# Kernel optimization log

Measured on AMD Instinct MI355X. Metric: run time of the kernel, lower is better.

The kernel has to match this reference:

```python
import jax, jax.numpy as jnp
import numpy as np

T, B, V, E, H = 128, 32, 32000, 32, 16
KEEP = 0.8  # 1 - dropout_percent


def setup_inputs() -> dict:
    key = jax.random.key(0)
    ks = jax.random.split(key, 11)
    stdv = 1.0 / np.sqrt(H)  # init_params: uniform(-stdv, stdv) for ALL params (incl. embedding)
    u = lambda k, shape: jax.random.uniform(k, shape, jnp.float32, -stdv, stdv)
    return {
        "input_batch": jax.random.randint(ks[0], (T, B), 0, V),
        "embedding": u(ks[1], (V, E)),
        "W_ih_lr": u(ks[2], (E + H, H)),
        "b_ih_lr": u(ks[3], (1, H)),
        "W_ih_rl": u(ks[4], (E + H, H)),
        "b_ih_rl": u(ks[5], (1, H)),
        "W_ho": u(ks[6], (2 * H, V)),
        "b_ho": u(ks[7], (1, V)),
        "initial_hidden": u(ks[8], (1, H)),
        # pre-sampled inverted-dropout masks (torch samples np.random.binomial each step)
        "mask_lr": jax.random.bernoulli(ks[9], KEEP, (T, B, H)).astype(jnp.float32) / KEEP,
        "mask_rl": jax.random.bernoulli(ks[10], KEEP, (T, B, H)).astype(jnp.float32) / KEEP,
    }


def reference(input_batch, embedding, W_ih_lr, b_ih_lr, W_ih_rl, b_ih_rl,
              W_ho, b_ho, initial_hidden, mask_lr, mask_rl):
    seq_len, batch = input_batch.shape
    # torch uses initial_hidden.data -> no grad flows into initial_hidden
    h0 = jnp.broadcast_to(jax.lax.stop_gradient(initial_hidden), (batch, initial_hidden.shape[1]))

    def make_step(W, b):
        def step(h, xm):
            ix, m = xm
            w = embedding[ix]                                   # [B, E] gather
            h = jnp.tanh(jnp.concatenate([w, h], axis=1) @ W + b) * m
            return h, h
        return step

    # left-to-right: hLR[t+1] = state after consuming token t
    _, ys_lr = jax.lax.scan(make_step(W_ih_lr, b_ih_lr), h0, (input_batch, mask_lr))
    # right-to-left: hRL[t-1] = state after consuming token t-1 (tokens fed reversed)
    _, ys_rl = jax.lax.scan(make_step(W_ih_rl, b_ih_rl), h0, (input_batch[::-1], mask_rl[::-1]))

    hLR = jnp.concatenate([h0[None], ys_lr], axis=0)        # [T+1, B, H]
    hRL = jnp.concatenate([ys_rl[::-1], h0[None]], axis=0)  # [T+1, B, H]

    # prediction for position i uses hLR[i] (left ctx) and hRL[i+1] (right ctx)
    feats = jnp.concatenate([hLR[:-1], hRL[1:]], axis=-1)   # [T, B, 2H]
    logits = feats @ W_ho + b_ho                            # [T, B, V]
    return jax.nn.log_softmax(logits, axis=-1)
```

## Files before the change

### kernel.cpp

```cpp
#include <hip/hip_runtime.h>
#include <hip/hip_bf16.h>
#include <math.h>

#define T_ 128
#define B_ 32
#define V_ 32000
#define E_ 32
#define H_ 16
#define NSEG 20
#define SEGW 1600
#define NIT 25

typedef __attribute__((ext_vector_type(8))) short short8;
typedef __attribute__((ext_vector_type(4))) float f32x4;


__global__ __launch_bounds__(256) void xw_kernel(const int* __restrict__ ix,
                                                 const float* __restrict__ emb,
                                                 const float* __restrict__ W_lr,
                                                 const float* __restrict__ b_lr,
                                                 const float* __restrict__ W_rl,
                                                 const float* __restrict__ b_rl,
                                                 float* __restrict__ xw) {
    int idx = blockIdx.x * 256 + threadIdx.x;
    int j = idx & 15;
    int b = (idx >> 4) & 31;
    int t = (idx >> 9) & 127;
    int dir = idx >> 16;
    const float* W    = dir ? W_rl : W_lr;
    const float* bias = dir ? b_rl : b_lr;
    int tok = ix[t * B_ + b];
    const float* er = emb + (long)tok * E_;
    float acc = bias[j];
#pragma unroll
    for (int e = 0; e < E_; ++e) acc += er[e] * W[e * H_ + j];
    xw[idx] = acc;
}

__global__ __launch_bounds__(512) void scan_kernel(const float* __restrict__ xw,
                                                   const float* __restrict__ W_lr,
                                                   const float* __restrict__ W_rl,
                                                   const float* __restrict__ h0p,
                                                   const float* __restrict__ mask_lr,
                                                   const float* __restrict__ mask_rl,
                                                   __hip_bfloat16* __restrict__ featsB) {
    int dir = blockIdx.x;
    int tid = threadIdx.x;
    int lane = tid & 63;
    int j = lane & 15;
    int b = tid >> 4;
    int base = lane & 48;
    const float* W    = dir ? W_rl : W_lr;
    const float* mask = dir ? mask_rl : mask_lr;
    const float* xwd  = xw + dir * (T_ * B_ * H_);
    float Wh[16];
#pragma unroll
    for (int k = 0; k < 16; ++k) Wh[k] = W[(E_ + k) * H_ + j];
    float h = h0p[j];
    if (dir == 0) featsB[(0 * B_ + b) * 32 + j] = __float2bfloat16(h);
    else          featsB[((T_ - 1) * B_ + b) * 32 + 16 + j] = __float2bfloat16(h);

    float x0[4], m0[4], x1[4], m1[4];
#define LOADCH(XB, MB, CH)                                                 \
    _Pragma("unroll")                                                      \
    for (int u = 0; u < 4; ++u) {                                          \
        int t = (CH) * 4 + u;                                              \
        int tt = dir ? (T_ - 1 - t) : t;                                   \
        XB[u] = xwd[tt * (B_ * H_) + tid];                                 \
        MB[u] = mask[tt * (B_ * H_) + tid];                                \
    }
#define STEPS(XB, MB, CH)                                                  \
    _Pragma("unroll")                                                      \
    for (int u = 0; u < 4; ++u) {                                          \
        int t = (CH) * 4 + u;                                              \
        float a0 = XB[u], a1 = 0.f, a2 = 0.f, a3 = 0.f;                    \
        _Pragma("unroll")                                                  \
        for (int k = 0; k < 16; k += 4) {                                  \
            a0 += __shfl(h, base + k,     64) * Wh[k];                     \
            a1 += __shfl(h, base + k + 1, 64) * Wh[k + 1];                 \
            a2 += __shfl(h, base + k + 2, 64) * Wh[k + 2];                 \
            a3 += __shfl(h, base + k + 3, 64) * Wh[k + 3];                 \
        }                                                                  \
        float ax = (a0 + a1) + (a2 + a3);                                  \
        float ex = __expf(2.f * ax);                                       \
        float th = 1.f - 2.f * __builtin_amdgcn_rcpf(ex + 1.f);            \
        float hn = th * MB[u];                                             \
        h = hn;                                                            \
        int p = dir ? (T_ - 2 - t) : (t + 1);                              \
        if (p >= 0 && p < T_)                                              \
            featsB[(p * B_ + b) * 32 + dir * 16 + j] = __float2bfloat16(hn); \
    }
    LOADCH(x0, m0, 0)
#pragma unroll 1
    for (int c = 0; c < 32; c += 2) {
        if (c + 1 < 32) { LOADCH(x1, m1, c + 1) }
        STEPS(x0, m0, c)
        if (c + 2 < 32) { LOADCH(x0, m0, c + 2) }
        STEPS(x1, m1, c + 1)
    }
#undef LOADCH
#undef STEPS
}

__global__ __launch_bounds__(256) void wt_kernel(const float* __restrict__ W_ho,
                                                 __hip_bfloat16* __restrict__ W_hoT) {
    int c = blockIdx.x * 256 + threadIdx.x;
    __hip_bfloat16 tmp[32];
#pragma unroll
    for (int k = 0; k < 32; ++k) tmp[k] = __float2bfloat16(W_ho[k * V_ + c]);
    short8* dst = (short8*)(W_hoT + c * 32);
    const short8* src = (const short8*)tmp;
#pragma unroll
    for (int q = 0; q < 4; ++q) dst[q] = src[q];
}


__global__ __launch_bounds__(256) void stats_kernel(const __hip_bfloat16* __restrict__ featsB,
                                                    const __hip_bfloat16* __restrict__ W_hoT,
                                                    const float* __restrict__ b_ho,
                                                    float* __restrict__ stats_part) {
    int wv = threadIdx.x >> 6, lane = threadIdx.x & 63;
    int rt = blockIdx.x * 4 + wv;
    int seg = blockIdx.y;
    int row0 = rt * 16;
    int p = lane & 15, kb = (lane >> 4) * 8, quad = (lane >> 4) << 2;
    short8 bfrag = *(const short8*)((const short*)featsB + (row0 + p) * 32 + kb);
    int cbase = seg * SEGW;
    const short* WA = (const short*)W_hoT;
    short8 a0n = *(const short8*)(WA + (cbase +  0 + p) * 32 + kb);
    short8 a1n = *(const short8*)(WA + (cbase + 16 + p) * 32 + kb);
    short8 a2n = *(const short8*)(WA + (cbase + 32 + p) * 32 + kb);
    short8 a3n = *(const short8*)(WA + (cbase + 48 + p) * 32 + kb);
    float r0 = 0.f, r1 = 0.f, r2 = 0.f, r3 = 0.f;
#pragma unroll 1
    for (int it = 0; it < NIT; ++it) {
        short8 a0 = a0n, a1 = a1n, a2 = a2n, a3 = a3n;
        if (it < NIT - 1) {
            int cn = cbase + (it + 1) * 64;
            a0n = *(const short8*)(WA + (cn +  0 + p) * 32 + kb);
            a1n = *(const short8*)(WA + (cn + 16 + p) * 32 + kb);
            a2n = *(const short8*)(WA + (cn + 32 + p) * 32 + kb);
            a3n = *(const short8*)(WA + (cn + 48 + p) * 32 + kb);
        }
        int c0 = cbase + it * 64;
        f32x4 b40 = *(const f32x4*)(b_ho + c0 +  0 + quad);
        f32x4 b41 = *(const f32x4*)(b_ho + c0 + 16 + quad);
        f32x4 b42 = *(const f32x4*)(b_ho + c0 + 32 + quad);
        f32x4 b43 = *(const f32x4*)(b_ho + c0 + 48 + quad);
        f32x4 lg0 = __builtin_amdgcn_mfma_f32_16x16x32_bf16(a0, bfrag, (f32x4){0.f,0.f,0.f,0.f}, 0, 0, 0);
        f32x4 lg1 = __builtin_amdgcn_mfma_f32_16x16x32_bf16(a1, bfrag, (f32x4){0.f,0.f,0.f,0.f}, 0, 0, 0);
        f32x4 lg2 = __builtin_amdgcn_mfma_f32_16x16x32_bf16(a2, bfrag, (f32x4){0.f,0.f,0.f,0.f}, 0, 0, 0);
        f32x4 lg3 = __builtin_amdgcn_mfma_f32_16x16x32_bf16(a3, bfrag, (f32x4){0.f,0.f,0.f,0.f}, 0, 0, 0);
        r0 += __expf(lg0[0] + b40[0]) + __expf(lg0[1] + b40[1]) +
              __expf(lg0[2] + b40[2]) + __expf(lg0[3] + b40[3]);
        r1 += __expf(lg1[0] + b41[0]) + __expf(lg1[1] + b41[1]) +
              __expf(lg1[2] + b41[2]) + __expf(lg1[3] + b41[3]);
        r2 += __expf(lg2[0] + b42[0]) + __expf(lg2[1] + b42[1]) +
              __expf(lg2[2] + b42[2]) + __expf(lg2[3] + b42[3]);
        r3 += __expf(lg3[0] + b43[0]) + __expf(lg3[1] + b43[1]) +
              __expf(lg3[2] + b43[2]) + __expf(lg3[3] + b43[3]);
    }
    float racc = (r0 + r1) + (r2 + r3);
    racc += __shfl_xor(racc, 16, 64);
    racc += __shfl_xor(racc, 32, 64);
    if (lane < 16) stats_part[(row0 + lane) * NSEG + seg] = racc;
}

__global__ __launch_bounds__(256) void lse_kernel(const float* __restrict__ stats_part,
                                                  float* __restrict__ lse) {
    int r = blockIdx.x * 256 + threadIdx.x;
    const float* sp = stats_part + r * NSEG;
    float s = 0.f;
#pragma unroll
    for (int i = 0; i < NSEG; ++i) s += sp[i];
    lse[r] = __logf(s);
}

__global__ __launch_bounds__(256) void out_kernel(const __hip_bfloat16* __restrict__ featsB,
                                                  const __hip_bfloat16* __restrict__ W_hoT,
                                                  const float* __restrict__ b_ho,
                                                  const float* __restrict__ lse,
                                                  float* __restrict__ out) {
    __shared__ float tile[4][16][68];
    int wv = threadIdx.x >> 6, lane = threadIdx.x & 63;
    int rt = blockIdx.x * 4 + wv;
    int seg = blockIdx.y;
    int row0 = rt * 16;
    int p = lane & 15, kb = (lane >> 4) * 8, quad = (lane >> 4) << 2;
    short8 bfrag = *(const short8*)((const short*)featsB + (row0 + p) * 32 + kb);
    float ls = lse[row0 + p];
    int cbase = seg * SEGW;
    const short* WA = (const short*)W_hoT;
    float* tw = &tile[wv][0][0];
    int rr = lane >> 4;
    int cc = (lane & 15) * 4;
    short8 a0n = *(const short8*)(WA + (cbase +  0 + p) * 32 + kb);
    short8 a1n = *(const short8*)(WA + (cbase + 16 + p) * 32 + kb);
    short8 a2n = *(const short8*)(WA + (cbase + 32 + p) * 32 + kb);
    short8 a3n = *(const short8*)(WA + (cbase + 48 + p) * 32 + kb);
#pragma unroll 1
    for (int it = 0; it < NIT; ++it) {
        short8 a0 = a0n, a1 = a1n, a2 = a2n, a3 = a3n;
        if (it < NIT - 1) {
            int cn = cbase + (it + 1) * 64;
            a0n = *(const short8*)(WA + (cn +  0 + p) * 32 + kb);
            a1n = *(const short8*)(WA + (cn + 16 + p) * 32 + kb);
            a2n = *(const short8*)(WA + (cn + 32 + p) * 32 + kb);
            a3n = *(const short8*)(WA + (cn + 48 + p) * 32 + kb);
        }
        int c0 = cbase + it * 64;
        f32x4 b40 = *(const f32x4*)(b_ho + c0 +  0 + quad);
        f32x4 b41 = *(const f32x4*)(b_ho + c0 + 16 + quad);
        f32x4 b42 = *(const f32x4*)(b_ho + c0 + 32 + quad);
        f32x4 b43 = *(const f32x4*)(b_ho + c0 + 48 + quad);
        f32x4 lg0 = __builtin_amdgcn_mfma_f32_16x16x32_bf16(a0, bfrag, (f32x4){0.f,0.f,0.f,0.f}, 0, 0, 0);
        f32x4 lg1 = __builtin_amdgcn_mfma_f32_16x16x32_bf16(a1, bfrag, (f32x4){0.f,0.f,0.f,0.f}, 0, 0, 0);
        f32x4 lg2 = __builtin_amdgcn_mfma_f32_16x16x32_bf16(a2, bfrag, (f32x4){0.f,0.f,0.f,0.f}, 0, 0, 0);
        f32x4 lg3 = __builtin_amdgcn_mfma_f32_16x16x32_bf16(a3, bfrag, (f32x4){0.f,0.f,0.f,0.f}, 0, 0, 0);
        *(f32x4*)(tw + p * 68 +  0 + quad) = lg0 + b40 - ls;
        *(f32x4*)(tw + p * 68 + 16 + quad) = lg1 + b41 - ls;
        *(f32x4*)(tw + p * 68 + 32 + quad) = lg2 + b42 - ls;
        *(f32x4*)(tw + p * 68 + 48 + quad) = lg3 + b43 - ls;
#pragma unroll
        for (int s = 0; s < 4; ++s) {
            int r = s * 4 + rr;
            f32x4 v = *(const f32x4*)(tw + r * 68 + cc);
            __builtin_nontemporal_store(v, (f32x4*)(out + (long)(row0 + r) * V_ + c0 + cc));
        }
    }
}

extern "C" void kernel_launch(void* const* d_in, const int* in_sizes, int n_in,
                              void* d_out, int out_size, void* d_ws, size_t ws_size,
                              hipStream_t stream) {
    const int*   ix      = (const int*)d_in[0];
    const float* emb     = (const float*)d_in[1];
    const float* W_lr    = (const float*)d_in[2];
    const float* b_lr    = (const float*)d_in[3];
    const float* W_rl    = (const float*)d_in[4];
    const float* b_rl    = (const float*)d_in[5];
    const float* W_ho    = (const float*)d_in[6];
    const float* b_ho    = (const float*)d_in[7];
    const float* h0      = (const float*)d_in[8];
    const float* mask_lr = (const float*)d_in[9];
    const float* mask_rl = (const float*)d_in[10];
    float* out = (float*)d_out;
    float* ws  = (float*)d_ws;

    float*           xw         = ws;
    __hip_bfloat16*  featsB     = (__hip_bfloat16*)(ws + 131072);
    __hip_bfloat16*  W_hoT      = (__hip_bfloat16*)(ws + 196608);
    float*           stats_part = ws + 708608;
    float*           lse        = ws + 790528;

    xw_kernel<<<512, 256, 0, stream>>>(ix, emb, W_lr, b_lr, W_rl, b_rl, xw);
    wt_kernel<<<125, 256, 0, stream>>>(W_ho, W_hoT);
    scan_kernel<<<2, 512, 0, stream>>>(xw, W_lr, W_rl, h0, mask_lr, mask_rl, featsB);
    stats_kernel<<<dim3(64, NSEG), 256, 0, stream>>>(featsB, W_hoT, b_ho, stats_part);
    lse_kernel<<<16, 256, 0, stream>>>(stats_part, lse);
    out_kernel<<<dim3(64, NSEG), 256, 0, stream>>>(featsB, W_hoT, b_ho, lse, out);
}
```

Before: 221.1 us.

## Split scan into per-wave blocks, fuse wt and lse, double rows in stats

The recurrent scan is split from 2 blocks of 512 threads into 16 single-wave blocks, one per direction and group of 4 batch rows, each run independently. The W_ho transpose runs as extra blocks of that same launch. The stats kernel now handles 32 rows per wave so each W_hoT fragment feeds two MFMAs. The lse kernel is removed: out_kernel sums the partial stats itself and stages the bias segment in shared memory. The intent is to cut launch count and serial latency in the scan, at the cost of redundant log-sum work in out_kernel and fewer stats blocks.

```diff
diff --git a/kernel.cpp b/kernel.cpp
--- a/kernel.cpp
+++ b/kernel.cpp
@@ -37,18 +37,31 @@
     xw[idx] = acc;
 }
 
-__global__ __launch_bounds__(512) void scan_kernel(const float* __restrict__ xw,
-                                                   const float* __restrict__ W_lr,
-                                                   const float* __restrict__ W_rl,
-                                                   const float* __restrict__ h0p,
-                                                   const float* __restrict__ mask_lr,
-                                                   const float* __restrict__ mask_rl,
-                                                   __hip_bfloat16* __restrict__ featsB) {
-    int dir = blockIdx.x;
-    int tid = threadIdx.x;
-    int lane = tid & 63;
+__global__ __launch_bounds__(64) void scanwt_kernel(const float* __restrict__ xw,
+                                                    const float* __restrict__ W_lr,
+                                                    const float* __restrict__ W_rl,
+                                                    const float* __restrict__ h0p,
+                                                    const float* __restrict__ mask_lr,
+                                                    const float* __restrict__ mask_rl,
+                                                    __hip_bfloat16* __restrict__ featsB,
+                                                    const float* __restrict__ W_ho,
+                                                    __hip_bfloat16* __restrict__ W_hoT) {
+    if (blockIdx.x >= 16) {
+        int c = (blockIdx.x - 16) * 64 + threadIdx.x;
+        __hip_bfloat16 tmp[32];
+#pragma unroll
+        for (int k = 0; k < 32; ++k) tmp[k] = __float2bfloat16(W_ho[k * V_ + c]);
+        short8* dst = (short8*)(W_hoT + c * 32);
+        const short8* src = (const short8*)tmp;
+#pragma unroll
+        for (int q = 0; q < 4; ++q) dst[q] = src[q];
+        return;
+    }
+    int lane = threadIdx.x;
+    int dir = blockIdx.x >> 3;
     int j = lane & 15;
-    int b = tid >> 4;
+    int b = (blockIdx.x & 7) * 4 + (lane >> 4);
+    int bi = b * 16 + j;
     int base = lane & 48;
     const float* W    = dir ? W_rl : W_lr;
     const float* mask = dir ? mask_rl : mask_lr;
@@ -66,8 +79,8 @@
     for (int u = 0; u < 4; ++u) {                                          \
         int t = (CH) * 4 + u;                                              \
         int tt = dir ? (T_ - 1 - t) : t;                                   \
-        XB[u] = xwd[tt * (B_ * H_) + tid];                                 \
-        MB[u] = mask[tt * (B_ * H_) + tid];                                \
+        XB[u] = xwd[tt * (B_ * H_) + bi];                                  \
+        MB[u] = mask[tt * (B_ * H_) + bi];                                 \
     }
 #define STEPS(XB, MB, CH)                                                  \
     _Pragma("unroll")                                                      \
@@ -102,18 +115,6 @@
 #undef STEPS
 }
 
-__global__ __launch_bounds__(256) void wt_kernel(const float* __restrict__ W_ho,
-                                                 __hip_bfloat16* __restrict__ W_hoT) {
-    int c = blockIdx.x * 256 + threadIdx.x;
-    __hip_bfloat16 tmp[32];
-#pragma unroll
-    for (int k = 0; k < 32; ++k) tmp[k] = __float2bfloat16(W_ho[k * V_ + c]);
-    short8* dst = (short8*)(W_hoT + c * 32);
-    const short8* src = (const short8*)tmp;
-#pragma unroll
-    for (int q = 0; q < 4; ++q) dst[q] = src[q];
-}
-
 
 __global__ __launch_bounds__(256) void stats_kernel(const __hip_bfloat16* __restrict__ featsB,
                                                     const __hip_bfloat16* __restrict__ W_hoT,
@@ -122,16 +123,17 @@
     int wv = threadIdx.x >> 6, lane = threadIdx.x & 63;
     int rt = blockIdx.x * 4 + wv;
     int seg = blockIdx.y;
-    int row0 = rt * 16;
+    int row0 = rt * 32;
     int p = lane & 15, kb = (lane >> 4) * 8, quad = (lane >> 4) << 2;
-    short8 bfrag = *(const short8*)((const short*)featsB + (row0 + p) * 32 + kb);
+    short8 bf0 = *(const short8*)((const short*)featsB + (row0 + p) * 32 + kb);
+    short8 bf1 = *(const short8*)((const short*)featsB + (row0 + 16 + p) * 32 + kb);
     int cbase = seg * SEGW;
     const short* WA = (const short*)W_hoT;
     short8 a0n = *(const short8*)(WA + (cbase +  0 + p) * 32 + kb);
     short8 a1n = *(const short8*)(WA + (cbase + 16 + p) * 32 + kb);
     short8 a2n = *(const short8*)(WA + (cbase + 32 + p) * 32 + kb);
     short8 a3n = *(const short8*)(WA + (cbase + 48 + p) * 32 + kb);
-    float r0 = 0.f, r1 = 0.f, r2 = 0.f, r3 = 0.f;
+    float ra = 0.f, rb = 0.f;
 #pragma unroll 1
     for (int it = 0; it < NIT; ++it) {
         short8 a0 = a0n, a1 = a1n, a2 = a2n, a3 = a3n;
@@ -147,49 +149,62 @@
         f32x4 b41 = *(const f32x4*)(b_ho + c0 + 16 + quad);
         f32x4 b42 = *(const f32x4*)(b_ho + c0 + 32 + quad);
         f32x4 b43 = *(const f32x4*)(b_ho + c0 + 48 + quad);
-        f32x4 lg0 = __builtin_amdgcn_mfma_f32_16x16x32_bf16(a0, bfrag, (f32x4){0.f,0.f,0.f,0.f}, 0, 0, 0);
-        f32x4 lg1 = __builtin_amdgcn_mfma_f32_16x16x32_bf16(a1, bfrag, (f32x4){0.f,0.f,0.f,0.f}, 0, 0, 0);
-        f32x4 lg2 = __builtin_amdgcn_mfma_f32_16x16x32_bf16(a2, bfrag, (f32x4){0.f,0.f,0.f,0.f}, 0, 0, 0);
-        f32x4 lg3 = __builtin_amdgcn_mfma_f32_16x16x32_bf16(a3, bfrag, (f32x4){0.f,0.f,0.f,0.f}, 0, 0, 0);
-        r0 += __expf(lg0[0] + b40[0]) + __expf(lg0[1] + b40[1]) +
-              __expf(lg0[2] + b40[2]) + __expf(lg0[3] + b40[3]);
-        r1 += __expf(lg1[0] + b41[0]) + __expf(lg1[1] + b41[1]) +
-              __expf(lg1[2] + b41[2]) + __expf(lg1[3] + b41[3]);
-        r2 += __expf(lg2[0] + b42[0]) + __expf(lg2[1] + b42[1]) +
-              __expf(lg2[2] + b42[2]) + __expf(lg2[3] + b42[3]);
-        r3 += __expf(lg3[0] + b43[0]) + __expf(lg3[1] + b43[1]) +
-              __expf(lg3[2] + b43[2]) + __expf(lg3[3] + b43[3]);
-    }
-    float racc = (r0 + r1) + (r2 + r3);
-    racc += __shfl_xor(racc, 16, 64);
-    racc += __shfl_xor(racc, 32, 64);
-    if (lane < 16) stats_part[(row0 + lane) * NSEG + seg] = racc;
-}
-
-__global__ __launch_bounds__(256) void lse_kernel(const float* __restrict__ stats_part,
-                                                  float* __restrict__ lse) {
-    int r = blockIdx.x * 256 + threadIdx.x;
-    const float* sp = stats_part + r * NSEG;
-    float s = 0.f;
-#pragma unroll
-    for (int i = 0; i < NSEG; ++i) s += sp[i];
-    lse[r] = __logf(s);
+        f32x4 la0 = __builtin_amdgcn_mfma_f32_16x16x32_bf16(a0, bf0, (f32x4){0.f,0.f,0.f,0.f}, 0, 0, 0);
+        f32x4 lb0 = __builtin_amdgcn_mfma_f32_16x16x32_bf16(a0, bf1, (f32x4){0.f,0.f,0.f,0.f}, 0, 0, 0);
+        f32x4 la1 = __builtin_amdgcn_mfma_f32_16x16x32_bf16(a1, bf0, (f32x4){0.f,0.f,0.f,0.f}, 0, 0, 0);
+        f32x4 lb1 = __builtin_amdgcn_mfma_f32_16x16x32_bf16(a1, bf1, (f32x4){0.f,0.f,0.f,0.f}, 0, 0, 0);
+        f32x4 la2 = __builtin_amdgcn_mfma_f32_16x16x32_bf16(a2, bf0, (f32x4){0.f,0.f,0.f,0.f}, 0, 0, 0);
+        f32x4 lb2 = __builtin_amdgcn_mfma_f32_16x16x32_bf16(a2, bf1, (f32x4){0.f,0.f,0.f,0.f}, 0, 0, 0);
+        f32x4 la3 = __builtin_amdgcn_mfma_f32_16x16x32_bf16(a3, bf0, (f32x4){0.f,0.f,0.f,0.f}, 0, 0, 0);
+        f32x4 lb3 = __builtin_amdgcn_mfma_f32_16x16x32_bf16(a3, bf1, (f32x4){0.f,0.f,0.f,0.f}, 0, 0, 0);
+        ra += __expf(la0[0] + b40[0]) + __expf(la0[1] + b40[1]) +
+              __expf(la0[2] + b40[2]) + __expf(la0[3] + b40[3]);
+        rb += __expf(lb0[0] + b40[0]) + __expf(lb0[1] + b40[1]) +
+              __expf(lb0[2] + b40[2]) + __expf(lb0[3] + b40[3]);
+        ra += __expf(la1[0] + b41[0]) + __expf(la1[1] + b41[1]) +
+              __expf(la1[2] + b41[2]) + __expf(la1[3] + b41[3]);
+        rb += __expf(lb1[0] + b41[0]) + __expf(lb1[1] + b41[1]) +
+              __expf(lb1[2] + b41[2]) + __expf(lb1[3] + b41[3]);
+        ra += __expf(la2[0] + b42[0]) + __expf(la2[1] + b42[1]) +
+              __expf(la2[2] + b42[2]) + __expf(la2[3] + b42[3]);
+        rb += __expf(lb2[0] + b42[0]) + __expf(lb2[1] + b42[1]) +
+              __expf(lb2[2] + b42[2]) + __expf(lb2[3] + b42[3]);
+        ra += __expf(la3[0] + b43[0]) + __expf(la3[1] + b43[1]) +
+              __expf(la3[2] + b43[2]) + __expf(la3[3] + b43[3]);
+        rb += __expf(lb3[0] + b43[0]) + __expf(lb3[1] + b43[1]) +
+              __expf(lb3[2] + b43[2]) + __expf(lb3[3] + b43[3]);
+    }
+    ra += __shfl_xor(ra, 16, 64);
+    ra += __shfl_xor(ra, 32, 64);
+    rb += __shfl_xor(rb, 16, 64);
+    rb += __shfl_xor(rb, 32, 64);
+    if (lane < 16) {
+        stats_part[(row0 + lane) * NSEG + seg] = ra;
+        stats_part[(row0 + 16 + lane) * NSEG + seg] = rb;
+    }
 }
 
 __global__ __launch_bounds__(256) void out_kernel(const __hip_bfloat16* __restrict__ featsB,
                                                   const __hip_bfloat16* __restrict__ W_hoT,
                                                   const float* __restrict__ b_ho,
-                                                  const float* __restrict__ lse,
+                                                  const float* __restrict__ stats_part,
                                                   float* __restrict__ out) {
     __shared__ float tile[4][16][68];
+    __shared__ float bseg[SEGW];
     int wv = threadIdx.x >> 6, lane = threadIdx.x & 63;
     int rt = blockIdx.x * 4 + wv;
     int seg = blockIdx.y;
     int row0 = rt * 16;
     int p = lane & 15, kb = (lane >> 4) * 8, quad = (lane >> 4) << 2;
+    int cbase = seg * SEGW;
+    for (int i = threadIdx.x; i < SEGW / 4; i += 256)
+        *(f32x4*)(bseg + i * 4) = *(const f32x4*)(b_ho + cbase + i * 4);
+    float s = 0.f;
+    const float* sp = stats_part + (row0 + p) * NSEG;
+#pragma unroll
+    for (int i = 0; i < NSEG; ++i) s += sp[i];
+    float ls = __logf(s);
     short8 bfrag = *(const short8*)((const short*)featsB + (row0 + p) * 32 + kb);
-    float ls = lse[row0 + p];
-    int cbase = seg * SEGW;
     const short* WA = (const short*)W_hoT;
     float* tw = &tile[wv][0][0];
     int rr = lane >> 4;
@@ -198,6 +213,7 @@
     short8 a1n = *(const short8*)(WA + (cbase + 16 + p) * 32 + kb);
     short8 a2n = *(const short8*)(WA + (cbase + 32 + p) * 32 + kb);
     short8 a3n = *(const short8*)(WA + (cbase + 48 + p) * 32 + kb);
+    __syncthreads();
 #pragma unroll 1
     for (int it = 0; it < NIT; ++it) {
         short8 a0 = a0n, a1 = a1n, a2 = a2n, a3 = a3n;
@@ -208,11 +224,11 @@
             a2n = *(const short8*)(WA + (cn + 32 + p) * 32 + kb);
             a3n = *(const short8*)(WA + (cn + 48 + p) * 32 + kb);
         }
-        int c0 = cbase + it * 64;
-        f32x4 b40 = *(const f32x4*)(b_ho + c0 +  0 + quad);
-        f32x4 b41 = *(const f32x4*)(b_ho + c0 + 16 + quad);
-        f32x4 b42 = *(const f32x4*)(b_ho + c0 + 32 + quad);
-        f32x4 b43 = *(const f32x4*)(b_ho + c0 + 48 + quad);
+        int co = it * 64;
+        f32x4 b40 = *(const f32x4*)(bseg + co +  0 + quad);
+        f32x4 b41 = *(const f32x4*)(bseg + co + 16 + quad);
+        f32x4 b42 = *(const f32x4*)(bseg + co + 32 + quad);
+        f32x4 b43 = *(const f32x4*)(bseg + co + 48 + quad);
         f32x4 lg0 = __builtin_amdgcn_mfma_f32_16x16x32_bf16(a0, bfrag, (f32x4){0.f,0.f,0.f,0.f}, 0, 0, 0);
         f32x4 lg1 = __builtin_amdgcn_mfma_f32_16x16x32_bf16(a1, bfrag, (f32x4){0.f,0.f,0.f,0.f}, 0, 0, 0);
         f32x4 lg2 = __builtin_amdgcn_mfma_f32_16x16x32_bf16(a2, bfrag, (f32x4){0.f,0.f,0.f,0.f}, 0, 0, 0);
@@ -221,9 +237,10 @@
         *(f32x4*)(tw + p * 68 + 16 + quad) = lg1 + b41 - ls;
         *(f32x4*)(tw + p * 68 + 32 + quad) = lg2 + b42 - ls;
         *(f32x4*)(tw + p * 68 + 48 + quad) = lg3 + b43 - ls;
-#pragma unroll
-        for (int s = 0; s < 4; ++s) {
-            int r = s * 4 + rr;
+        int c0 = cbase + co;
+#pragma unroll
+        for (int sN = 0; sN < 4; ++sN) {
+            int r = sN * 4 + rr;
             f32x4 v = *(const f32x4*)(tw + r * 68 + cc);
             __builtin_nontemporal_store(v, (f32x4*)(out + (long)(row0 + r) * V_ + c0 + cc));
         }
@@ -251,12 +268,10 @@
     __hip_bfloat16*  featsB     = (__hip_bfloat16*)(ws + 131072);
     __hip_bfloat16*  W_hoT      = (__hip_bfloat16*)(ws + 196608);
     float*           stats_part = ws + 708608;
-    float*           lse        = ws + 790528;
 
     xw_kernel<<<512, 256, 0, stream>>>(ix, emb, W_lr, b_lr, W_rl, b_rl, xw);
-    wt_kernel<<<125, 256, 0, stream>>>(W_ho, W_hoT);
-    scan_kernel<<<2, 512, 0, stream>>>(xw, W_lr, W_rl, h0, mask_lr, mask_rl, featsB);
-    stats_kernel<<<dim3(64, NSEG), 256, 0, stream>>>(featsB, W_hoT, b_ho, stats_part);
-    lse_kernel<<<16, 256, 0, stream>>>(stats_part, lse);
-    out_kernel<<<dim3(64, NSEG), 256, 0, stream>>>(featsB, W_hoT, b_ho, lse, out);
-}
+    scanwt_kernel<<<516, 64, 0, stream>>>(xw, W_lr, W_rl, h0, mask_lr, mask_rl,
+                                          featsB, W_ho, W_hoT);
+    stats_kernel<<<dim3(32, NSEG), 256, 0, stream>>>(featsB, W_hoT, b_ho, stats_part);
+    out_kernel<<<dim3(64, NSEG), 256, 0, stream>>>(featsB, W_hoT, b_ho, stats_part, out);
+}
```

New measurement: 182.0 us. 1.22x faster.
